# Kernel tuning notes

Hardware: AMD Instinct MI355X
Metric: run time of the kernel (lower is better)

The kernel has to match this reference:

```python
import jax, jax.numpy as jnp
import numpy as np

DIM = 512
N_SLOTS = 32
B, T = 32, 2048


def entmax15(z):
    """Entmax-1.5 along last axis (exact sort-based algorithm of Peters et al.)."""
    z = z / 2.0
    z = z - jnp.max(z, axis=-1, keepdims=True)
    zs = jnp.flip(jnp.sort(z, axis=-1), axis=-1)          # descending
    n = z.shape[-1]
    k = jnp.arange(1, n + 1, dtype=z.dtype)
    mean = jnp.cumsum(zs, axis=-1) / k
    mean_sq = jnp.cumsum(zs * zs, axis=-1) / k
    ss = k * (mean_sq - mean * mean)
    delta = jnp.clip((1.0 - ss) / k, 0.0)
    tau = mean - jnp.sqrt(delta)
    support = (tau <= zs).astype(jnp.int32)
    k_star = jnp.sum(support, axis=-1, keepdims=True) - 1  # last supported index
    tau_star = jnp.take_along_axis(tau, k_star, axis=-1)
    p = jnp.clip(z - tau_star, 0.0)
    return p * p


def setup_inputs() -> dict:
    key = jax.random.key(0)
    k1, k2, k3, k4 = jax.random.split(key, 4)
    scale = 1.0 / np.sqrt(DIM)
    return {
        "x_seq": jax.random.normal(k1, (B, T, DIM), jnp.float32),
        "h_tape": jnp.zeros((B, N_SLOTS, DIM), jnp.float32),
        "h_work": jnp.zeros((B, DIM), jnp.float32),
        "W_h": jax.random.normal(k2, (DIM, DIM), jnp.float32) * scale * 0.9,
        "W_x": jax.random.normal(k3, (DIM, DIM), jnp.float32) * scale,
        "b_h": jnp.zeros((DIM,), jnp.float32),
        "W_write": jax.random.normal(k4, (DIM, DIM), jnp.float32) * scale,
    }


def reference(x_seq, h_tape, h_work, W_h, W_x, b_h, W_write):
    D = x_seq.shape[-1]
    inv_sqrt_d = 1.0 / jnp.sqrt(jnp.asarray(D, x_seq.dtype))

    def step(carry, x_t):
        tape, work = carry                                   # [B,N,D], [B,D]
        # entmax read addressing keyed by working memory
        r_scores = jnp.einsum('bnd,bd->bn', tape, work) * inv_sqrt_d
        alpha = entmax15(r_scores)
        read = jnp.einsum('bn,bnd->bd', alpha, tape)
        # Elman-style working memory update
        work_new = jnp.tanh(work @ W_h.T + x_t @ W_x.T + read + b_h)
        # entmax write addressing, convex slot update
        w_vec = work_new @ W_write.T
        w_scores = jnp.einsum('bnd,bd->bn', tape, w_vec) * inv_sqrt_d
        beta = entmax15(w_scores)[..., None]                 # [B,N,1]
        tape_new = tape * (1.0 - beta) + beta * w_vec[:, None, :]
        return (tape_new, work_new), work_new

    (tape_final, _), h_seq = jax.lax.scan(
        step, (h_tape, h_work), jnp.swapaxes(x_seq, 0, 1))
    h_seq = jnp.swapaxes(h_seq, 0, 1)                        # [B,T,D]
    return h_seq, tape_final, h_seq[:, -1]
```

## Files before the change

### kernel.cpp

```cpp
#include <hip/hip_runtime.h>
#include <math.h>

#define DIM 512
#define NSLOTS 32
#define BATCH 32
#define SEQT 2048
#define KSPLIT 8
#define SLICE 64
#define TPB 512
#define TPAD 68

#define SCOPE_AGENT __HIP_MEMORY_SCOPE_AGENT

__global__ __launch_bounds__(256) void xw_gemm_kernel(
    const float* __restrict__ A,
    const float* __restrict__ Bm,
    const float* __restrict__ bias,
    float* __restrict__ C)
{
    __shared__ __align__(16) float As[16][68];
    __shared__ __align__(16) float Bs[16][68];

    const int tid = threadIdx.x;
    const int tx = tid & 15, ty = tid >> 4;
    const int bm = blockIdx.x, bo = blockIdx.y;
    const int r = tid >> 2, c = tid & 3;

    float acc[4][4];
#pragma unroll
    for (int i = 0; i < 4; ++i)
#pragma unroll
        for (int j = 0; j < 4; ++j) acc[i][j] = 0.f;

    const float* Arow = A + (size_t)(bm * 64 + r) * DIM + c * 4;
    const float* Brow = Bm + (size_t)(bo * 64 + r) * DIM + c * 4;

    for (int kt = 0; kt < DIM / 16; ++kt) {
        float4 a4 = *(const float4*)(Arow + kt * 16);
        float4 b4 = *(const float4*)(Brow + kt * 16);
        As[c * 4 + 0][r] = a4.x; As[c * 4 + 1][r] = a4.y;
        As[c * 4 + 2][r] = a4.z; As[c * 4 + 3][r] = a4.w;
        Bs[c * 4 + 0][r] = b4.x; Bs[c * 4 + 1][r] = b4.y;
        Bs[c * 4 + 2][r] = b4.z; Bs[c * 4 + 3][r] = b4.w;
        __syncthreads();
#pragma unroll
        for (int kk = 0; kk < 16; ++kk) {
            float4 av = *(const float4*)&As[kk][ty * 4];
            float4 bv = *(const float4*)&Bs[kk][tx * 4];
            float a[4] = {av.x, av.y, av.z, av.w};
            float b[4] = {bv.x, bv.y, bv.z, bv.w};
#pragma unroll
            for (int i = 0; i < 4; ++i)
#pragma unroll
                for (int j = 0; j < 4; ++j)
                    acc[i][j] = fmaf(a[i], b[j], acc[i][j]);
        }
        __syncthreads();
    }

    const int col = bo * 64 + tx * 4;
    float4 bia = *(const float4*)(bias + col);
#pragma unroll
    for (int i = 0; i < 4; ++i) {
        float4 v = {acc[i][0] + bia.x, acc[i][1] + bia.y,
                    acc[i][2] + bia.z, acc[i][3] + bia.w};
        *(float4*)(C + (size_t)(bm * 64 + ty * 4 + i) * DIM + col) = v;
    }
}

__device__ __forceinline__ float entmax_wave(float sc, int lane)
{
    float z = sc * 0.5f;
    float zmax = z;
#pragma unroll
    for (int off = 16; off >= 1; off >>= 1)
        zmax = fmaxf(zmax, __shfl_xor(zmax, off, 32));
    z -= zmax;
    int rank = 0;
#pragma unroll
    for (int j = 0; j < 32; ++j) {
        float zj = __shfl(z, j, 32);
        rank += (zj > z) || (zj == z && j < lane);
    }
    float zsv = __int_as_float(
        __builtin_amdgcn_ds_permute(rank << 2, __float_as_int(z)));
    float cs = zsv, css = zsv * zsv;
#pragma unroll
    for (int off = 1; off < 32; off <<= 1) {
        float a = __shfl_up(cs, off, 32);
        float b2 = __shfl_up(css, off, 32);
        if (lane >= off) { cs += a; css += b2; }
    }
    float kk = (float)(lane + 1);
    float mean = cs / kk, meansq = css / kk;
    float ss = kk * (meansq - mean * mean);
    float delta = fmaxf((1.0f - ss) / kk, 0.0f);
    float tau = mean - sqrtf(delta);
    unsigned long long ball = __ballot(tau <= zsv);
    int kstar = __popcll(ball & 0xFFFFFFFFull) - 1;
    float taustar = __shfl(tau, kstar, 32);
    float pp = fmaxf(z - taustar, 0.0f);
    return pp * pp;
}

union f2u { float2 f; unsigned long long u; };

__device__ __forceinline__ void wg_sync(int* cnt_b, int target, int* deadflag,
                                        int tid)
{
    if (tid == 0 && !*deadflag) {
        __hip_atomic_fetch_add(cnt_b, 1, __ATOMIC_RELAXED, SCOPE_AGENT);
        int it = 0;
        while (__hip_atomic_load(cnt_b, __ATOMIC_RELAXED, SCOPE_AGENT) <
               target) {
            if (++it > (1 << 20)) { *deadflag = 1; break; }
            if (it > 8) __builtin_amdgcn_s_sleep(2);
        }
    }
    __syncthreads();
}

__global__ __launch_bounds__(TPB) void recurrent_kernel(
    const float* __restrict__ h_tape0,
    const float* __restrict__ h_work0,
    const float* __restrict__ W_h,
    const float* __restrict__ W_write,
    float* out,
    unsigned long long* partsM,
    unsigned long long* partsA,
    int* cnt)
{
    __shared__ __align__(16) float tape[NSLOTS][TPAD];
    __shared__ __align__(16) float wkF[SLICE];
    __shared__ __align__(16) float wvF[SLICE];
    __shared__ __align__(16) float m1F[SLICE];
    __shared__ __align__(16) float2 probBA[NSLOTS];
    __shared__ int deadflag;

    const int tid = threadIdx.x;
    const int bid = blockIdx.x;
    const int k = bid & 7;
    const int b = bid >> 3;
    const float inv_sqrt_d = 0.044194173824159216f;

    float4 w1r[16], w2r[16];
    {
        const float4* Wh = (const float4*)(W_h + (size_t)tid * DIM + k * SLICE);
        const float4* Ww = (const float4*)(W_write + (size_t)tid * DIM + k * SLICE);
#pragma unroll
        for (int j = 0; j < 16; ++j) { w1r[j] = Wh[j]; w2r[j] = Ww[j]; }
    }

    if (tid == 0) deadflag = 0;
    {
        const int n = tid >> 4, c4 = tid & 15;
        float4 tv = *(const float4*)(h_tape0 +
            ((size_t)(b * NSLOTS + n)) * DIM + k * SLICE + 4 * c4);
        *(float4*)&tape[n][4 * c4] = tv;
    }
    if (tid < SLICE) {
        wkF[tid] = h_work0[b * DIM + k * SLICE + tid];
        wvF[tid] = 0.f;
        m1F[tid] = 0.f;
    }
    __syncthreads();

    float* hseq_b = out + (size_t)b * SEQT * DIM;
    int* cnt_b = cnt + b * 32;
    unsigned long long* pM = partsM + (size_t)b * KSPLIT * DIM;
    unsigned long long* pA = partsA + (size_t)b * KSPLIT * 33;

    {
        const float4* wk4 = (const float4*)wkF;
        float m1 = 0.f, m2 = 0.f;
#pragma unroll
        for (int j = 0; j < 16; ++j) {
            float4 wv = wk4[j];
            m1 = fmaf(w1r[j].x, wv.x, m1); m1 = fmaf(w1r[j].y, wv.y, m1);
            m1 = fmaf(w1r[j].z, wv.z, m1); m1 = fmaf(w1r[j].w, wv.w, m1);
            m2 = fmaf(w2r[j].x, wv.x, m2); m2 = fmaf(w2r[j].y, wv.y, m2);
            m2 = fmaf(w2r[j].z, wv.z, m2); m2 = fmaf(w2r[j].w, wv.w, m2);
        }
        f2u v; v.f = make_float2(m1, m2);
        __hip_atomic_store(&pM[k * DIM + tid], v.u, __ATOMIC_RELAXED,
                           SCOPE_AGENT);
        asm volatile("s_waitcnt vmcnt(0)" ::: "memory");
        __syncthreads();
        wg_sync(cnt_b, KSPLIT, &deadflag, tid);
        if (tid < SLICE) {
            float a1 = 0.f, a2 = 0.f;
#pragma unroll
            for (int j = 0; j < KSPLIT; ++j) {
                f2u v2;
                v2.u = __hip_atomic_load(&pM[j * DIM + k * SLICE + tid],
                                         __ATOMIC_RELAXED, SCOPE_AGENT);
                a1 += v2.f.x; a2 += v2.f.y;
            }
            m1F[tid] = a1;
            wvF[tid] = a2;
        }
        __syncthreads();
    }

    for (int t = 0; t < SEQT; ++t) {
        float xv = 0.f;
        if ((tid & 7) == 0)
            xv = hseq_b[(size_t)t * DIM + k * SLICE + (tid >> 3)];

        {
            const int s = tid >> 4, l = tid & 15;
            float4 tv = *(const float4*)&tape[s][4 * l];
            float4 wv = *(const float4*)&wvF[4 * l];
            float4 wk = *(const float4*)&wkF[4 * l];
            float up = tv.x * wv.x;
            up = fmaf(tv.y, wv.y, up); up = fmaf(tv.z, wv.z, up);
            up = fmaf(tv.w, wv.w, up);
            float vp = tv.x * wk.x;
            vp = fmaf(tv.y, wk.y, vp); vp = fmaf(tv.z, wk.z, vp);
            vp = fmaf(tv.w, wk.w, vp);
#pragma unroll
            for (int off = 8; off >= 1; off >>= 1) {
                up += __shfl_down(up, off, 16);
                vp += __shfl_down(vp, off, 16);
            }
            if (l == 0) {
                f2u v; v.f = make_float2(up, vp);
                __hip_atomic_store(&pA[k * 33 + s], v.u, __ATOMIC_RELAXED,
                                   SCOPE_AGENT);
            }
            if (tid < 16) {
                float4 a = *(const float4*)&wvF[4 * tid];
                float4 b4 = *(const float4*)&wkF[4 * tid];
                float sp = a.x * b4.x;
                sp = fmaf(a.y, b4.y, sp); sp = fmaf(a.z, b4.z, sp);
                sp = fmaf(a.w, b4.w, sp);
#pragma unroll
                for (int off = 8; off >= 1; off >>= 1)
                    sp += __shfl_down(sp, off, 16);
                if (tid == 0) {
                    f2u v; v.f = make_float2(sp, 0.f);
                    __hip_atomic_store(&pA[k * 33 + 32], v.u, __ATOMIC_RELAXED,
                                       SCOPE_AGENT);
                }
            }
        }
        asm volatile("s_waitcnt vmcnt(0)" ::: "memory");
        __syncthreads();
        wg_sync(cnt_b, (2 * t + 2) * KSPLIT, &deadflag, tid);

        if (tid < 64) {
            float uu = 0.f, vv = 0.f;
            if (tid < 33) {
#pragma unroll
                for (int j = 0; j < KSPLIT; ++j) {
                    f2u v2;
                    v2.u = __hip_atomic_load(&pA[j * 33 + tid],
                                             __ATOMIC_RELAXED, SCOPE_AGENT);
                    uu += v2.f.x; vv += v2.f.y;
                }
            }
            float sfull = __shfl(uu, 32);
            if (tid < 32) {
                float beta = 0.f;
                if (t > 0) beta = entmax_wave(uu * inv_sqrt_d, tid);
                float rr = ((1.0f - beta) * vv + beta * sfull) * inv_sqrt_d;
                float alpha = entmax_wave(rr, tid);
                probBA[tid] = make_float2(beta, alpha);
            }
        }
        __syncthreads();

        {
            const int n = tid >> 4, c4 = tid & 15;
            float bb = probBA[n].x;
            if (bb != 0.f) {
                float4 tv = *(const float4*)&tape[n][4 * c4];
                float4 wv = *(const float4*)&wvF[4 * c4];
                tv.x = tv.x * (1.0f - bb) + bb * wv.x;
                tv.y = tv.y * (1.0f - bb) + bb * wv.y;
                tv.z = tv.z * (1.0f - bb) + bb * wv.z;
                tv.w = tv.w * (1.0f - bb) + bb * wv.w;
                *(float4*)&tape[n][4 * c4] = tv;
            }
        }
        __syncthreads();

        {
            const int c = tid >> 3, j = tid & 7;
            float p = 0.f;
#pragma unroll
            for (int i = 0; i < 4; ++i) {
                int n = 4 * j + i;
                p = fmaf(probBA[n].y, tape[n][c], p);
            }
            p += __shfl_down(p, 4, 8);
            p += __shfl_down(p, 2, 8);
            p += __shfl_down(p, 1, 8);
            if (j == 0) {
                float wn = tanhf(m1F[c] + xv + p);
                wkF[c] = wn;
                hseq_b[(size_t)t * DIM + k * SLICE + c] = wn;
            }
        }
        __syncthreads();

        {
            const float4* wk4 = (const float4*)wkF;
            float m1 = 0.f, m2 = 0.f;
#pragma unroll
            for (int j = 0; j < 16; ++j) {
                float4 wv = wk4[j];
                m1 = fmaf(w1r[j].x, wv.x, m1); m1 = fmaf(w1r[j].y, wv.y, m1);
                m1 = fmaf(w1r[j].z, wv.z, m1); m1 = fmaf(w1r[j].w, wv.w, m1);
                m2 = fmaf(w2r[j].x, wv.x, m2); m2 = fmaf(w2r[j].y, wv.y, m2);
                m2 = fmaf(w2r[j].z, wv.z, m2); m2 = fmaf(w2r[j].w, wv.w, m2);
            }
            f2u v; v.f = make_float2(m1, m2);
            __hip_atomic_store(&pM[k * DIM + tid], v.u, __ATOMIC_RELAXED,
                               SCOPE_AGENT);
        }
        asm volatile("s_waitcnt vmcnt(0)" ::: "memory");
        __syncthreads();
        wg_sync(cnt_b, (2 * t + 3) * KSPLIT, &deadflag, tid);

        if (tid < SLICE) {
            float a1 = 0.f, a2 = 0.f;
#pragma unroll
            for (int j = 0; j < KSPLIT; ++j) {
                f2u v2;
                v2.u = __hip_atomic_load(&pM[j * DIM + k * SLICE + tid],
                                         __ATOMIC_RELAXED, SCOPE_AGENT);
                a1 += v2.f.x; a2 += v2.f.y;
            }
            m1F[tid] = a1;
            wvF[tid] = a2;
        }
        __syncthreads();
    }

    {
        const int s = tid >> 4, l = tid & 15;
        float4 tv = *(const float4*)&tape[s][4 * l];
        float4 wv = *(const float4*)&wvF[4 * l];
        float up = tv.x * wv.x;
        up = fmaf(tv.y, wv.y, up); up = fmaf(tv.z, wv.z, up);
        up = fmaf(tv.w, wv.w, up);
#pragma unroll
        for (int off = 8; off >= 1; off >>= 1)
            up += __shfl_down(up, off, 16);
        if (l == 0) {
            f2u v; v.f = make_float2(up, 0.f);
            __hip_atomic_store(&pA[k * 33 + s], v.u, __ATOMIC_RELAXED,
                               SCOPE_AGENT);
        }
    }
    asm volatile("s_waitcnt vmcnt(0)" ::: "memory");
    __syncthreads();
    wg_sync(cnt_b, (2 * SEQT + 2) * KSPLIT, &deadflag, tid);
    if (tid < 32) {
        float uu = 0.f;
#pragma unroll
        for (int j = 0; j < KSPLIT; ++j) {
            f2u v2;
            v2.u = __hip_atomic_load(&pA[j * 33 + tid], __ATOMIC_RELAXED,
                                     SCOPE_AGENT);
            uu += v2.f.x;
        }
        float beta = entmax_wave(uu * inv_sqrt_d, tid);
        probBA[tid] = make_float2(beta, 0.f);
    }
    __syncthreads();
    {
        const int n = tid >> 4, c4 = tid & 15;
        float bb = probBA[n].x;
        if (bb != 0.f) {
            float4 tv = *(const float4*)&tape[n][4 * c4];
            float4 wv = *(const float4*)&wvF[4 * c4];
            tv.x = tv.x * (1.0f - bb) + bb * wv.x;
            tv.y = tv.y * (1.0f - bb) + bb * wv.y;
            tv.z = tv.z * (1.0f - bb) + bb * wv.z;
            tv.w = tv.w * (1.0f - bb) + bb * wv.w;
            *(float4*)&tape[n][4 * c4] = tv;
        }
    }
    __syncthreads();

    {
        const int n = tid >> 4, c4 = tid & 15;
        float4 tv = *(const float4*)&tape[n][4 * c4];
        *(float4*)(out + (size_t)BATCH * SEQT * DIM +
                   ((size_t)(b * NSLOTS + n)) * DIM + k * SLICE + 4 * c4) = tv;
    }
    if (tid < SLICE)
        out[(size_t)BATCH * SEQT * DIM + (size_t)BATCH * NSLOTS * DIM +
            (size_t)b * DIM + k * SLICE + tid] = wkF[tid];
}

extern "C" void kernel_launch(void* const* d_in, const int* in_sizes, int n_in,
                              void* d_out, int out_size, void* d_ws,
                              size_t ws_size, hipStream_t stream)
{
    const float* x_seq   = (const float*)d_in[0];
    const float* h_tape  = (const float*)d_in[1];
    const float* h_work  = (const float*)d_in[2];
    const float* W_h     = (const float*)d_in[3];
    const float* W_x     = (const float*)d_in[4];
    const float* b_h     = (const float*)d_in[5];
    const float* W_write = (const float*)d_in[6];
    float* out = (float*)d_out;

    unsigned long long* partsM = (unsigned long long*)d_ws;
    unsigned long long* partsA = partsM + (size_t)BATCH * KSPLIT * DIM;
    int* cnt = (int*)(partsA + (size_t)BATCH * KSPLIT * 33);

    hipMemsetAsync(cnt, 0, BATCH * 32 * sizeof(int), stream);

    dim3 g1((BATCH * SEQT) / 64, DIM / 64);
    xw_gemm_kernel<<<g1, 256, 0, stream>>>(x_seq, W_x, b_h, out);

    recurrent_kernel<<<BATCH * KSPLIT, TPB, 0, stream>>>(
        h_tape, h_work, W_h, W_write, out, partsM, partsA, cnt);
}
```

Before: 16.44 ms.

## Replace counter barrier with per-block tags, transpose tape, fuse tape update into read

```diff
diff --git a/kernel.cpp b/kernel.cpp
--- a/kernel.cpp
+++ b/kernel.cpp
@@ -8,9 +8,9 @@
 #define KSPLIT 8
 #define SLICE 64
 #define TPB 512
-#define TPAD 68
 
 #define SCOPE_AGENT __HIP_MEMORY_SCOPE_AGENT
+#define SCOPE_WG    __HIP_MEMORY_SCOPE_WORKGROUP
 
 __global__ __launch_bounds__(256) void xw_gemm_kernel(
     const float* __restrict__ A,
@@ -68,56 +68,67 @@
     }
 }
 
-__device__ __forceinline__ float entmax_wave(float sc, int lane)
+__device__ __forceinline__ float entmax64(float sc, int lane)
 {
-    float z = sc * 0.5f;
+    const int slot = lane & 31;
+    float z = __shfl(sc, slot, 64) * 0.5f;
     float zmax = z;
 #pragma unroll
     for (int off = 16; off >= 1; off >>= 1)
-        zmax = fmaxf(zmax, __shfl_xor(zmax, off, 32));
+        zmax = fmaxf(zmax, __shfl_xor(zmax, off, 64));
     z -= zmax;
+    const int jbase = (lane & 32) >> 1;
     int rank = 0;
 #pragma unroll
-    for (int j = 0; j < 32; ++j) {
-        float zj = __shfl(z, j, 32);
-        rank += (zj > z) || (zj == z && j < lane);
-    }
-    float zsv = __int_as_float(
-        __builtin_amdgcn_ds_permute(rank << 2, __float_as_int(z)));
-    float cs = zsv, css = zsv * zsv;
-#pragma unroll
-    for (int off = 1; off < 32; off <<= 1) {
-        float a = __shfl_up(cs, off, 32);
-        float b2 = __shfl_up(css, off, 32);
-        if (lane >= off) { cs += a; css += b2; }
-    }
-    float kk = (float)(lane + 1);
-    float mean = cs / kk, meansq = css / kk;
-    float ss = kk * (meansq - mean * mean);
-    float delta = fmaxf((1.0f - ss) / kk, 0.0f);
-    float tau = mean - sqrtf(delta);
-    unsigned long long ball = __ballot(tau <= zsv);
-    int kstar = __popcll(ball & 0xFFFFFFFFull) - 1;
-    float taustar = __shfl(tau, kstar, 32);
-    float pp = fmaxf(z - taustar, 0.0f);
-    return pp * pp;
+    for (int j = 0; j < 16; ++j) {
+        int jj = jbase + j;
+        float zj = __shfl(z, jj, 64);
+        rank += (zj > z) || (zj == z && jj < slot);
+    }
+    rank += __shfl_xor(rank, 32, 64);
+    float pp = 0.f;
+    if (lane < 32) {
+        float zsv = __int_as_float(
+            __builtin_amdgcn_ds_permute(rank << 2, __float_as_int(z)));
+        float cs = zsv, css = zsv * zsv;
+#pragma unroll
+        for (int off = 1; off < 32; off <<= 1) {
+            float a = __shfl_up(cs, off, 32);
+            float b2 = __shfl_up(css, off, 32);
+            if (lane >= off) { cs += a; css += b2; }
+        }
+        float kk = (float)(lane + 1);
+        float mean = cs / kk, meansq = css / kk;
+        float ss = kk * (meansq - mean * mean);
+        float delta = fmaxf((1.0f - ss) / kk, 0.0f);
+        float tau = mean - sqrtf(delta);
+        unsigned long long ball = __ballot(tau <= zsv);
+        int kstar = __popcll(ball & 0xFFFFFFFFull) - 1;
+        float taustar = __shfl(tau, kstar, 32);
+        pp = fmaxf(z - taustar, 0.0f);
+        pp = pp * pp;
+    }
+    return pp;
 }
 
 union f2u { float2 f; unsigned long long u; };
 
-__device__ __forceinline__ void wg_sync(int* cnt_b, int target, int* deadflag,
-                                        int tid)
+__device__ __forceinline__ void poll8(int* tags, int target, int* dead,
+                                      int lane)
 {
-    if (tid == 0 && !*deadflag) {
-        __hip_atomic_fetch_add(cnt_b, 1, __ATOMIC_RELAXED, SCOPE_AGENT);
+    bool d = __hip_atomic_load(dead, __ATOMIC_RELAXED, SCOPE_WG) != 0;
+    if (lane < KSPLIT && !d) {
         int it = 0;
-        while (__hip_atomic_load(cnt_b, __ATOMIC_RELAXED, SCOPE_AGENT) <
+        while (__hip_atomic_load(&tags[lane], __ATOMIC_RELAXED, SCOPE_AGENT) <
                target) {
-            if (++it > (1 << 20)) { *deadflag = 1; break; }
-            if (it > 8) __builtin_amdgcn_s_sleep(2);
-        }
-    }
-    __syncthreads();
+            if (++it > (1 << 20)) {
+                __hip_atomic_store(dead, 1, __ATOMIC_RELAXED, SCOPE_WG);
+                break;
+            }
+            __builtin_amdgcn_s_sleep(1);
+        }
+    }
+    asm volatile("" ::: "memory");
 }
 
 __global__ __launch_bounds__(TPB) void recurrent_kernel(
@@ -128,9 +139,10 @@
     float* out,
     unsigned long long* partsM,
     unsigned long long* partsA,
-    int* cnt)
+    int* tagA,
+    int* tagM)
 {
-    __shared__ __align__(16) float tape[NSLOTS][TPAD];
+    __shared__ __align__(16) float tape_t[SLICE][NSLOTS + 1];
     __shared__ __align__(16) float wkF[SLICE];
     __shared__ __align__(16) float wvF[SLICE];
     __shared__ __align__(16) float m1F[SLICE];
@@ -156,7 +168,10 @@
         const int n = tid >> 4, c4 = tid & 15;
         float4 tv = *(const float4*)(h_tape0 +
             ((size_t)(b * NSLOTS + n)) * DIM + k * SLICE + 4 * c4);
-        *(float4*)&tape[n][4 * c4] = tv;
+        tape_t[4 * c4 + 0][n] = tv.x;
+        tape_t[4 * c4 + 1][n] = tv.y;
+        tape_t[4 * c4 + 2][n] = tv.z;
+        tape_t[4 * c4 + 3][n] = tv.w;
     }
     if (tid < SLICE) {
         wkF[tid] = h_work0[b * DIM + k * SLICE + tid];
@@ -166,9 +181,10 @@
     __syncthreads();
 
     float* hseq_b = out + (size_t)b * SEQT * DIM;
-    int* cnt_b = cnt + b * 32;
     unsigned long long* pM = partsM + (size_t)b * KSPLIT * DIM;
     unsigned long long* pA = partsA + (size_t)b * KSPLIT * 33;
+    int* tagA_b = tagA + b * 32;
+    int* tagM_b = tagM + b * 32;
 
     {
         const float4* wk4 = (const float4*)wkF;
@@ -186,8 +202,10 @@
                            SCOPE_AGENT);
         asm volatile("s_waitcnt vmcnt(0)" ::: "memory");
         __syncthreads();
-        wg_sync(cnt_b, KSPLIT, &deadflag, tid);
-        if (tid < SLICE) {
+        if (tid == 0)
+            __hip_atomic_store(&tagM_b[k], 1, __ATOMIC_RELAXED, SCOPE_AGENT);
+        if (tid < 64) {
+            poll8(tagM_b, 1, &deadflag, tid);
             float a1 = 0.f, a2 = 0.f;
 #pragma unroll
             for (int j = 0; j < KSPLIT; ++j) {
@@ -198,57 +216,52 @@
             }
             m1F[tid] = a1;
             wvF[tid] = a2;
-        }
-        __syncthreads();
+            asm volatile("s_waitcnt lgkmcnt(0)" ::: "memory");
+        }
     }
 
     for (int t = 0; t < SEQT; ++t) {
         float xv = 0.f;
-        if ((tid & 7) == 0)
+        if (tid >= 64 && (tid & 7) == 0)
             xv = hseq_b[(size_t)t * DIM + k * SLICE + (tid >> 3)];
 
-        {
-            const int s = tid >> 4, l = tid & 15;
-            float4 tv = *(const float4*)&tape[s][4 * l];
-            float4 wv = *(const float4*)&wvF[4 * l];
-            float4 wk = *(const float4*)&wkF[4 * l];
-            float up = tv.x * wv.x;
-            up = fmaf(tv.y, wv.y, up); up = fmaf(tv.z, wv.z, up);
-            up = fmaf(tv.w, wv.w, up);
-            float vp = tv.x * wk.x;
-            vp = fmaf(tv.y, wk.y, vp); vp = fmaf(tv.z, wk.z, vp);
-            vp = fmaf(tv.w, wk.w, vp);
-#pragma unroll
-            for (int off = 8; off >= 1; off >>= 1) {
-                up += __shfl_down(up, off, 16);
-                vp += __shfl_down(vp, off, 16);
-            }
-            if (l == 0) {
+        if (tid < 64) {
+            const int s2 = tid >> 1, h = tid & 1;
+            float up = 0.f, vp = 0.f, sp = 0.f;
+#pragma unroll
+            for (int m = 0; m < 8; ++m) {
+                const int c0 = 32 * h + 4 * m;
+                float4 wv = *(const float4*)&wvF[c0];
+                float4 wk = *(const float4*)&wkF[c0];
+                float t0 = tape_t[c0 + 0][s2], t1 = tape_t[c0 + 1][s2];
+                float t2 = tape_t[c0 + 2][s2], t3 = tape_t[c0 + 3][s2];
+                up = fmaf(t0, wv.x, up); up = fmaf(t1, wv.y, up);
+                up = fmaf(t2, wv.z, up); up = fmaf(t3, wv.w, up);
+                vp = fmaf(t0, wk.x, vp); vp = fmaf(t1, wk.y, vp);
+                vp = fmaf(t2, wk.z, vp); vp = fmaf(t3, wk.w, vp);
+                sp = fmaf(wv.x, wk.x, sp); sp = fmaf(wv.y, wk.y, sp);
+                sp = fmaf(wv.z, wk.z, sp); sp = fmaf(wv.w, wk.w, sp);
+            }
+            up += __shfl_down(up, 1, 2);
+            vp += __shfl_down(vp, 1, 2);
+            sp += __shfl_down(sp, 1, 2);
+            if (h == 0) {
                 f2u v; v.f = make_float2(up, vp);
-                __hip_atomic_store(&pA[k * 33 + s], v.u, __ATOMIC_RELAXED,
+                __hip_atomic_store(&pA[k * 33 + s2], v.u, __ATOMIC_RELAXED,
                                    SCOPE_AGENT);
             }
-            if (tid < 16) {
-                float4 a = *(const float4*)&wvF[4 * tid];
-                float4 b4 = *(const float4*)&wkF[4 * tid];
-                float sp = a.x * b4.x;
-                sp = fmaf(a.y, b4.y, sp); sp = fmaf(a.z, b4.z, sp);
-                sp = fmaf(a.w, b4.w, sp);
-#pragma unroll
-                for (int off = 8; off >= 1; off >>= 1)
-                    sp += __shfl_down(sp, off, 16);
-                if (tid == 0) {
-                    f2u v; v.f = make_float2(sp, 0.f);
-                    __hip_atomic_store(&pA[k * 33 + 32], v.u, __ATOMIC_RELAXED,
-                                       SCOPE_AGENT);
-                }
-            }
-        }
-        asm volatile("s_waitcnt vmcnt(0)" ::: "memory");
-        __syncthreads();
-        wg_sync(cnt_b, (2 * t + 2) * KSPLIT, &deadflag, tid);
-
-        if (tid < 64) {
+            if (tid == 0) {
+                f2u v; v.f = make_float2(sp, 0.f);
+                __hip_atomic_store(&pA[k * 33 + 32], v.u, __ATOMIC_RELAXED,
+                                   SCOPE_AGENT);
+            }
+            asm volatile("s_waitcnt vmcnt(0)" ::: "memory");
+            if (tid == 0)
+                __hip_atomic_store(&tagA_b[k], t + 1, __ATOMIC_RELAXED,
+                                   SCOPE_AGENT);
+            if ((tid & 7) == 0)
+                xv = hseq_b[(size_t)t * DIM + k * SLICE + (tid >> 3)];
+            poll8(tagA_b, t + 1, &deadflag, tid);
             float uu = 0.f, vv = 0.f;
             if (tid < 33) {
 #pragma unroll
@@ -259,45 +272,33 @@
                     uu += v2.f.x; vv += v2.f.y;
                 }
             }
-            float sfull = __shfl(uu, 32);
-            if (tid < 32) {
-                float beta = 0.f;
-                if (t > 0) beta = entmax_wave(uu * inv_sqrt_d, tid);
-                float rr = ((1.0f - beta) * vv + beta * sfull) * inv_sqrt_d;
-                float alpha = entmax_wave(rr, tid);
-                probBA[tid] = make_float2(beta, alpha);
-            }
-        }
-        __syncthreads();
-
-        {
-            const int n = tid >> 4, c4 = tid & 15;
-            float bb = probBA[n].x;
-            if (bb != 0.f) {
-                float4 tv = *(const float4*)&tape[n][4 * c4];
-                float4 wv = *(const float4*)&wvF[4 * c4];
-                tv.x = tv.x * (1.0f - bb) + bb * wv.x;
-                tv.y = tv.y * (1.0f - bb) + bb * wv.y;
-                tv.z = tv.z * (1.0f - bb) + bb * wv.z;
-                tv.w = tv.w * (1.0f - bb) + bb * wv.w;
-                *(float4*)&tape[n][4 * c4] = tv;
-            }
+            float sfull = __shfl(uu, 32, 64);
+            float beta = 0.f;
+            if (t > 0) beta = entmax64(uu * inv_sqrt_d, tid);
+            float rr = ((1.0f - beta) * vv + beta * sfull) * inv_sqrt_d;
+            float alpha = entmax64(rr, tid);
+            if (tid < 32) probBA[tid] = make_float2(beta, alpha);
         }
         __syncthreads();
 
         {
             const int c = tid >> 3, j = tid & 7;
-            float p = 0.f;
+            float wvc = wvF[c];
+            float racc = 0.f;
 #pragma unroll
             for (int i = 0; i < 4; ++i) {
                 int n = 4 * j + i;
-                p = fmaf(probBA[n].y, tape[n][c], p);
-            }
-            p += __shfl_down(p, 4, 8);
-            p += __shfl_down(p, 2, 8);
-            p += __shfl_down(p, 1, 8);
+                float2 ba = probBA[n];
+                float tv = tape_t[c][n];
+                tv = tv * (1.0f - ba.x) + ba.x * wvc;
+                tape_t[c][n] = tv;
+                racc = fmaf(ba.y, tv, racc);
+            }
+            racc += __shfl_down(racc, 4, 8);
+            racc += __shfl_down(racc, 2, 8);
+            racc += __shfl_down(racc, 1, 8);
             if (j == 0) {
-                float wn = tanhf(m1F[c] + xv + p);
+                float wn = tanhf(m1F[c] + xv + racc);
                 wkF[c] = wn;
                 hseq_b[(size_t)t * DIM + k * SLICE + c] = wn;
             }
@@ -321,9 +322,11 @@
         }
         asm volatile("s_waitcnt vmcnt(0)" ::: "memory");
         __syncthreads();
-        wg_sync(cnt_b, (2 * t + 3) * KSPLIT, &deadflag, tid);
-
-        if (tid < SLICE) {
+        if (tid == 0)
+            __hip_atomic_store(&tagM_b[k], t + 2, __ATOMIC_RELAXED,
+                               SCOPE_AGENT);
+        if (tid < 64) {
+            poll8(tagM_b, t + 2, &deadflag, tid);
             float a1 = 0.f, a2 = 0.f;
 #pragma unroll
             for (int j = 0; j < KSPLIT; ++j) {
@@ -334,60 +337,64 @@
             }
             m1F[tid] = a1;
             wvF[tid] = a2;
-        }
-        __syncthreads();
-    }
-
-    {
-        const int s = tid >> 4, l = tid & 15;
-        float4 tv = *(const float4*)&tape[s][4 * l];
-        float4 wv = *(const float4*)&wvF[4 * l];
-        float up = tv.x * wv.x;
-        up = fmaf(tv.y, wv.y, up); up = fmaf(tv.z, wv.z, up);
-        up = fmaf(tv.w, wv.w, up);
-#pragma unroll
-        for (int off = 8; off >= 1; off >>= 1)
-            up += __shfl_down(up, off, 16);
-        if (l == 0) {
+            asm volatile("s_waitcnt lgkmcnt(0)" ::: "memory");
+        }
+    }
+
+    if (tid < 64) {
+        const int s2 = tid >> 1, h = tid & 1;
+        float up = 0.f;
+#pragma unroll
+        for (int m = 0; m < 8; ++m) {
+            const int c0 = 32 * h + 4 * m;
+            float4 wv = *(const float4*)&wvF[c0];
+            up = fmaf(tape_t[c0 + 0][s2], wv.x, up);
+            up = fmaf(tape_t[c0 + 1][s2], wv.y, up);
+            up = fmaf(tape_t[c0 + 2][s2], wv.z, up);
+            up = fmaf(tape_t[c0 + 3][s2], wv.w, up);
+        }
+        up += __shfl_down(up, 1, 2);
+        if (h == 0) {
             f2u v; v.f = make_float2(up, 0.f);
-            __hip_atomic_store(&pA[k * 33 + s], v.u, __ATOMIC_RELAXED,
+            __hip_atomic_store(&pA[k * 33 + s2], v.u, __ATOMIC_RELAXED,
                                SCOPE_AGENT);
         }
-    }
-    asm volatile("s_waitcnt vmcnt(0)" ::: "memory");
-    __syncthreads();
-    wg_sync(cnt_b, (2 * SEQT + 2) * KSPLIT, &deadflag, tid);
-    if (tid < 32) {
+        asm volatile("s_waitcnt vmcnt(0)" ::: "memory");
+        if (tid == 0)
+            __hip_atomic_store(&tagA_b[k], SEQT + 1, __ATOMIC_RELAXED,
+                               SCOPE_AGENT);
+        poll8(tagA_b, SEQT + 1, &deadflag, tid);
         float uu = 0.f;
-#pragma unroll
-        for (int j = 0; j < KSPLIT; ++j) {
-            f2u v2;
-            v2.u = __hip_atomic_load(&pA[j * 33 + tid], __ATOMIC_RELAXED,
-                                     SCOPE_AGENT);
-            uu += v2.f.x;
-        }
-        float beta = entmax_wave(uu * inv_sqrt_d, tid);
-        probBA[tid] = make_float2(beta, 0.f);
+        if (tid < 32) {
+#pragma unroll
+            for (int j = 0; j < KSPLIT; ++j) {
+                f2u v2;
+                v2.u = __hip_atomic_load(&pA[j * 33 + tid], __ATOMIC_RELAXED,
+                                         SCOPE_AGENT);
+                uu += v2.f.x;
+            }
+        }
+        float beta = entmax64(uu * inv_sqrt_d, tid);
+        if (tid < 32) probBA[tid] = make_float2(beta, 0.f);
     }
     __syncthreads();
     {
-        const int n = tid >> 4, c4 = tid & 15;
-        float bb = probBA[n].x;
-        if (bb != 0.f) {
-            float4 tv = *(const float4*)&tape[n][4 * c4];
-            float4 wv = *(const float4*)&wvF[4 * c4];
-            tv.x = tv.x * (1.0f - bb) + bb * wv.x;
-            tv.y = tv.y * (1.0f - bb) + bb * wv.y;
-            tv.z = tv.z * (1.0f - bb) + bb * wv.z;
-            tv.w = tv.w * (1.0f - bb) + bb * wv.w;
-            *(float4*)&tape[n][4 * c4] = tv;
+        const int c = tid >> 3, j = tid & 7;
+        float wvc = wvF[c];
+#pragma unroll
+        for (int i = 0; i < 4; ++i) {
+            int n = 4 * j + i;
+            float bb = probBA[n].x;
+            float tv = tape_t[c][n];
+            tape_t[c][n] = tv * (1.0f - bb) + bb * wvc;
         }
     }
     __syncthreads();
 
     {
         const int n = tid >> 4, c4 = tid & 15;
-        float4 tv = *(const float4*)&tape[n][4 * c4];
+        float4 tv = {tape_t[4 * c4 + 0][n], tape_t[4 * c4 + 1][n],
+                     tape_t[4 * c4 + 2][n], tape_t[4 * c4 + 3][n]};
         *(float4*)(out + (size_t)BATCH * SEQT * DIM +
                    ((size_t)(b * NSLOTS + n)) * DIM + k * SLICE + 4 * c4) = tv;
     }
@@ -411,13 +418,14 @@
 
     unsigned long long* partsM = (unsigned long long*)d_ws;
     unsigned long long* partsA = partsM + (size_t)BATCH * KSPLIT * DIM;
-    int* cnt = (int*)(partsA + (size_t)BATCH * KSPLIT * 33);
-
-    hipMemsetAsync(cnt, 0, BATCH * 32 * sizeof(int), stream);
+    int* tagA = (int*)(partsA + (size_t)BATCH * KSPLIT * 33);
+    int* tagM = tagA + BATCH * 32;
+
+    hipMemsetAsync(tagA, 0, 2 * BATCH * 32 * sizeof(int), stream);
 
     dim3 g1((BATCH * SEQT) / 64, DIM / 64);
     xw_gemm_kernel<<<g1, 256, 0, stream>>>(x_seq, W_x, b_h, out);
 
     recurrent_kernel<<<BATCH * KSPLIT, TPB, 0, stream>>>(
-        h_tape, h_work, W_h, W_write, out, partsM, partsA, cnt);
+        h_tape, h_work, W_h, W_write, out, partsM, partsA, tagA, tagM);
 }
```

New measurement: 14.37 ms. 12.6% less time.
